# Kernel optimization log

Measured on AMD Instinct MI355X. Metric: run time of the kernel, lower is better.

## Reference

```python
import jax, jax.numpy as jnp
import numpy as np


def _matfun(X, f):
    """Apply scalar function f to eigenvalues of symmetric X (batched)."""
    Xs = 0.5 * (X + jnp.swapaxes(X, -1, -2))
    s, U = jnp.linalg.eigh(Xs)
    return jnp.einsum('...ij,...j,...kj->...ik', U, f(s), U)


def _invsqrtm(M):
    return _matfun(M, lambda s: 1.0 / jnp.sqrt(s))


def _sqrtm(M):
    return _matfun(M, jnp.sqrt)


def _logm(M):
    return _matfun(M, jnp.log)


def _expm(M):
    return _matfun(M, jnp.exp)


def _powm(M, p):
    return _matfun(M, lambda s: s ** p)


def setup_inputs() -> dict:
    key = jax.random.key(0)
    B, n = 2048, 128
    A = jax.random.normal(key, (B, n, n), dtype=jnp.float32)
    # SPD inputs: A A^T / n + 0.5 I (well conditioned, distinct eigenvalues)
    X = A @ jnp.swapaxes(A, -1, -2) / n + 0.5 * jnp.eye(n, dtype=jnp.float32)
    mean = jnp.eye(n, dtype=jnp.float32)          # self.mean (learn_mean=False)
    running_mean = jnp.eye(n, dtype=jnp.float32)  # running_mean buffer
    return {"X": X, "mean": mean, "running_mean": running_mean}


def reference(X, mean, running_mean):
    """SPDBatchNorm.forward, training mode, dispersion=False, batchdim=0."""
    karcher_steps = 1
    eta = 1.0
    sg = jax.lax.stop_gradient

    # Karcher flow to the batch Frechet mean
    batch_mean = X.mean(axis=0, keepdims=True)            # (1, n, n)
    for _ in range(karcher_steps):
        bm_invsqrt = _invsqrtm(sg(batch_mean))            # detach, as in torch
        X_proj = _logm(bm_invsqrt @ X @ bm_invsqrt)       # (B, n, n)
        bm_proj = X_proj.mean(axis=0, keepdims=True)
        bm_sqrt = _sqrtm(sg(batch_mean))
        batch_mean = bm_sqrt @ _expm(bm_proj) @ bm_sqrt

    # geodesic update of running mean toward batch mean (weight eta)
    rm_invsqrt = _invsqrtm(running_mean)
    power = _powm(rm_invsqrt @ batch_mean @ rm_invsqrt, eta)
    rm_sqrt = _sqrtm(running_mean)
    running_mean_new = rm_sqrt @ power @ rm_sqrt          # (1, n, n)

    # transp_via_identity(X, S=running_mean_new, T=mean):
    #   sqrt(T) @ invsqrt(S) @ X @ invsqrt(S) @ sqrt(T)
    S_invsqrt = _invsqrtm(running_mean_new)
    T_sqrt = _sqrtm(mean)
    Xn = T_sqrt @ (S_invsqrt @ X @ S_invsqrt) @ T_sqrt
    return Xn
```

## Files before the change

kernel.cpp:

```cpp
#include <hip/hip_runtime.h>

typedef _Float16 f16;
typedef _Float16 f16x8 __attribute__((ext_vector_type(8)));
typedef _Float16 f16x4 __attribute__((ext_vector_type(4)));
typedef float    f32x4 __attribute__((ext_vector_type(4)));

#define NN 16384

#define CHM 1.9f
#define CHH 1.6f
__device__ __constant__ float CB[14] = {
   0.6418302f,  0.8422835f, -0.3523330f,  0.1927408f,
  -0.1587888f,  0.1475312f,  0.1189440f, -0.2249536f,
  -0.4700032f,  0.5836800f,  0.4901376f, -0.5607424f,
  -0.2453504f,  0.2477460f };

__device__ __forceinline__ int swz(int r, int c) {
  return (r << 7) + ((((c >> 3) ^ (r & 7)) << 3) | (c & 7));
}

__device__ __forceinline__ void load_g2l_h(const f16* __restrict__ G, f16* buf, int t, int nt) {
  for (int ch = t; ch < 2048; ch += nt) {
    int r = ch >> 4, c8 = (ch & 15) << 3;
    *(f16x8*)(buf + swz(r, c8)) = *(const f16x8*)(G + (r << 7) + c8);
  }
}

__device__ __forceinline__ void stage32_512(const f16* __restrict__ src, f16* dst, int t) {
  const int w = t >> 6, l = t & 63;
  #pragma unroll
  for (int q = 0; q < 4; ++q) {
    const int cb = (w * 4 + q) * 64;
    __builtin_amdgcn_global_load_lds(
        (const __attribute__((address_space(1))) unsigned int*)(src + (size_t)(cb + l) * 8),
        (__attribute__((address_space(3))) unsigned int*)((char*)dst + (size_t)cb * 16), 16, 0, 0);
  }
}
__device__ __forceinline__ void stage32_256(const f16* __restrict__ src, f16* dst, int t) {
  const int w = t >> 6, l = t & 63;
  #pragma unroll
  for (int q = 0; q < 8; ++q) {
    const int cb = (w * 8 + q) * 64;
    __builtin_amdgcn_global_load_lds(
        (const __attribute__((address_space(1))) unsigned int*)(src + (size_t)(cb + l) * 8),
        (__attribute__((address_space(3))) unsigned int*)((char*)dst + (size_t)cb * 16), 16, 0, 0);
  }
}

template<int NI>
__device__ __forceinline__ void zero_acc(f32x4 (&acc)[NI][4]) {
  #pragma unroll
  for (int i = 0; i < NI; ++i)
    #pragma unroll
    for (int j = 0; j < 4; ++j) acc[i][j] = (f32x4){0.f, 0.f, 0.f, 0.f};
}

template<int NI>
__device__ __forceinline__ void mm_lds(const f16* A, const f16* Bh,
                                       f32x4 (&acc)[NI][4], int w, int l) {
  const int tr0 = (w >> 1) * (16 * NI), tc0 = (w & 1) * 64;
  #pragma unroll
  for (int ks = 0; ks < 4; ++ks) {
    const int kb = ks * 32 + ((l >> 4) << 3);
    f16x8 af[NI], bf[4];
    #pragma unroll
    for (int i = 0; i < NI; ++i) af[i] = *(const f16x8*)(A  + swz(tr0 + i*16 + (l & 15), kb));
    #pragma unroll
    for (int j = 0; j < 4; ++j) bf[j] = *(const f16x8*)(Bh + swz(tc0 + j*16 + (l & 15), kb));
    #pragma unroll
    for (int i = 0; i < NI; ++i)
      #pragma unroll
      for (int j = 0; j < 4; ++j)
        acc[i][j] = __builtin_amdgcn_mfma_f32_16x16x32_f16(af[i], bf[j], acc[i][j], 0, 0, 0);
  }
}

template<int NI>
__device__ __forceinline__ void mm_pre(const f16* A, const f16x8* bfr,
                                       f32x4 (&acc)[NI][4], int w, int l) {
  const int tr0 = (w >> 1) * (16 * NI);
  #pragma unroll
  for (int ks = 0; ks < 4; ++ks) {
    const int kb = ks * 32 + ((l >> 4) << 3);
    f16x8 af[NI];
    #pragma unroll
    for (int i = 0; i < NI; ++i) af[i] = *(const f16x8*)(A + swz(tr0 + i*16 + (l & 15), kb));
    #pragma unroll
    for (int i = 0; i < NI; ++i)
      #pragma unroll
      for (int j = 0; j < 4; ++j)
        acc[i][j] = __builtin_amdgcn_mfma_f32_16x16x32_f16(af[i], bfr[ks*4+j], acc[i][j], 0, 0, 0);
  }
}
__device__ __forceinline__ void pre_bf_gswz(const f16* __restrict__ B, f16x8* bfr, int w, int l) {
  const int tc0 = (w & 1) * 64;
  #pragma unroll
  for (int ks = 0; ks < 4; ++ks) {
    const int kb = ks * 32 + ((l >> 4) << 3);
    #pragma unroll
    for (int j = 0; j < 4; ++j)
      bfr[ks*4+j] = *(const f16x8*)(B + swz(tc0 + j*16 + (l & 15), kb));
  }
}
template<int NI>
__device__ __forceinline__ void pre_chunks(const f16* M, f16x4* Cc, int w, int l) {
  const int tr0 = (w >> 1) * (16 * NI), tc0 = (w & 1) * 64;
  #pragma unroll
  for (int i = 0; i < NI; ++i) {
    const int rowb = tr0 + i*16 + ((l >> 4) << 2);
    #pragma unroll
    for (int j = 0; j < 4; ++j)
      Cc[i*4+j] = *(const f16x4*)(M + swz(tc0 + j*16 + (l & 15), rowb));
  }
}

template<int NI>
__device__ __forceinline__ void wb_t(f16* buf, const f32x4 (&acc)[NI][4], int w, int l,
                                     float alpha, float beta) {
  const int tr0 = (w >> 1) * (16 * NI), tc0 = (w & 1) * 64;
  #pragma unroll
  for (int i = 0; i < NI; ++i) {
    const int rowb = tr0 + i*16 + ((l >> 4) << 2);
    #pragma unroll
    for (int j = 0; j < 4; ++j) {
      const int colg = tc0 + j*16 + (l & 15);
      f16x4 h;
      #pragma unroll
      for (int r = 0; r < 4; ++r) {
        float v = alpha * acc[i][j][r];
        if (rowb + r == colg) v += beta;
        h[r] = (f16)v;
      }
      *(f16x4*)(buf + swz(colg, rowb)) = h;
    }
  }
}

template<int NI>
__device__ __forceinline__ void wb_t_split(f16* bh, f16* bl, const f32x4 (&acc)[NI][4],
                                           int w, int l) {
  const int tr0 = (w >> 1) * (16 * NI), tc0 = (w & 1) * 64;
  #pragma unroll
  for (int i = 0; i < NI; ++i) {
    const int rowb = tr0 + i*16 + ((l >> 4) << 2);
    #pragma unroll
    for (int j = 0; j < 4; ++j) {
      const int colg = tc0 + j*16 + (l & 15);
      f16x4 hh, hl;
      #pragma unroll
      for (int r = 0; r < 4; ++r) {
        float v = acc[i][j][r];
        f16 hi = (f16)v;
        hh[r] = hi; hl[r] = (f16)(v - (float)hi);
      }
      *(f16x4*)(bh + swz(colg, rowb)) = hh;
      *(f16x4*)(bl + swz(colg, rowb)) = hl;
    }
  }
}

template<int NI>
__device__ __forceinline__ void wb_t_combo3L(f16* buf, const f32x4 (&acc)[NI][4],
                                             const f16x4* Uc, const f16x4* U2c, const f16* C3,
                                             int w, int l, float d0, float d1, float d2, float d3) {
  const int tr0 = (w >> 1) * (16 * NI), tc0 = (w & 1) * 64;
  #pragma unroll
  for (int i = 0; i < NI; ++i) {
    const int rowb = tr0 + i*16 + ((l >> 4) << 2);
    #pragma unroll
    for (int j = 0; j < 4; ++j) {
      const int colg = tc0 + j*16 + (l & 15);
      f16x4 c3 = *(const f16x4*)(C3 + swz(colg, rowb));
      f16x4 h;
      #pragma unroll
      for (int r = 0; r < 4; ++r) {
        float v = acc[i][j][r] + d1 * (float)Uc[i*4+j][r] + d2 * (float)U2c[i*4+j][r]
                               + d3 * (float)c3[r];
        if (rowb + r == colg) v += d0;
        h[r] = (f16)v;
      }
      *(f16x4*)(buf + swz(colg, rowb)) = h;
    }
  }
}

template<int NI>
__device__ __forceinline__ void wb_t_gc(f16* buf, const f32x4 (&acc)[NI][4],
                                        const f16* C1, const f16* C2,
                                        int w, int l, float d0, float d1, float d2) {
  const int tr0 = (w >> 1) * (16 * NI), tc0 = (w & 1) * 64;
  #pragma unroll
  for (int i = 0; i < NI; ++i) {
    const int rowb = tr0 + i*16 + ((l >> 4) << 2);
    #pragma unroll
    for (int j = 0; j < 4; ++j) {
      const int colg = tc0 + j*16 + (l & 15);
      f16x4 c1 = *(const f16x4*)(C1 + swz(colg, rowb));
      f16x4 c2 = *(const f16x4*)(C2 + swz(colg, rowb));
      f16x4 h;
      #pragma unroll
      for (int r = 0; r < 4; ++r) {
        float v = acc[i][j][r] + d1 * (float)c1[r] + d2 * (float)c2[r];
        if (rowb + r == colg) v += d0;
        h[r] = (f16)v;
      }
      *(f16x4*)(buf + swz(colg, rowb)) = h;
    }
  }
}

__global__ void k_mean_part(const float* __restrict__ X, f16* __restrict__ Xh,
                            float* __restrict__ part, int nper) {
  const int ch = blockIdx.x * 256 + threadIdx.x;
  const int bc = blockIdx.y;
  const int r = ch >> 4, c8 = (ch & 15) << 3;
  const int dsw = swz(r, c8);
  const float* p = X + (size_t)bc * nper * NN + (size_t)ch * 8;
  f16* xh = Xh + (size_t)bc * nper * NN + dsw;
  f32x4 s0 = {0.f,0.f,0.f,0.f}, s1 = {0.f,0.f,0.f,0.f};
  for (int b = 0; b < nper; ++b) {
    const float* g = p + (size_t)b * NN;
    f32x4 v0 = *(const f32x4*)g;
    f32x4 v1 = *(const f32x4*)(g + 4);
    s0 = s0 + v0; s1 = s1 + v1;
    f16x8 h;
    h[0]=(f16)v0[0]; h[1]=(f16)v0[1]; h[2]=(f16)v0[2]; h[3]=(f16)v0[3];
    h[4]=(f16)v1[0]; h[5]=(f16)v1[1]; h[6]=(f16)v1[2]; h[7]=(f16)v1[3];
    *(f16x8*)(xh + (size_t)b * NN) = h;
  }
  f32x4* pp = (f32x4*)(part + (size_t)bc * NN);
  pp[ch * 2]     = s0;
  pp[ch * 2 + 1] = s1;
}
__global__ void k_mean_fin(const float* __restrict__ part, float* __restrict__ M0, float scale) {
  int e4 = blockIdx.x * 256 + threadIdx.x;
  f32x4 s = {0.f,0.f,0.f,0.f};
  for (int c = 0; c < 32; ++c) s = s + ((const f32x4*)part)[(size_t)c * 4096 + e4];
  ((f32x4*)M0)[e4] = s * scale;
}

__global__ __launch_bounds__(512) void kB(
    const float* __restrict__ M0, f16* __restrict__ Cps,
    f16* __restrict__ Rh, f16* __restrict__ Rl) {
  __shared__ __align__(16) f16 A1[NN], A2[NN], A3[NN], A4[NN];
  __shared__ float red[128];
  __shared__ float sS;
  const int t = threadIdx.x, w = t >> 6, l = t & 63;
  if (t < 128) red[t] = M0[t * 129];
  __syncthreads();
  for (int s = 64; s > 0; s >>= 1) { if (t < s) red[t] += red[t + s]; __syncthreads(); }
  if (t == 0) sS = red[0] / 128.f;
  __syncthreads();
  const float s = sS, inv = 1.f / s;
  for (int e = t; e < NN; e += 512) {
    int r = e >> 7, c = e & 127;
    A1[swz(r, c)] = (f16)(M0[e] * inv - (r == c ? 1.f : 0.f));
  }
  __syncthreads();
  f32x4 acc[2][4];
  zero_acc<2>(acc); mm_lds<2>(A1, A1, acc, w, l); wb_t<2>(A2, acc, w, l, 1.f, 0.f); __syncthreads();
  zero_acc<2>(acc); mm_lds<2>(A2, A1, acc, w, l); wb_t<2>(A3, acc, w, l, 1.f, 0.f); __syncthreads();
  zero_acc<2>(acc); mm_lds<2>(A2, A2, acc, w, l); wb_t<2>(A4, acc, w, l, 1.f, 0.f); __syncthreads();
  const float rs = sqrtf(s), irs = 1.f / rs;
  for (int e = t; e < NN; e += 512) {
    int r = e >> 7, c = e & 127; int ix = swz(r, c);
    float a1 = (float)A1[ix], a2 = (float)A2[ix], a3 = (float)A3[ix], a4 = (float)A4[ix];
    float d = (r == c) ? 1.f : 0.f;
    float cp = (d - 0.5f*a1 + 0.375f*a2 - 0.3125f*a3 + 0.2734375f*a4) * irs;
    float rr = (d + 0.5f*a1 - 0.125f*a2 + 0.0625f*a3 - 0.0390625f*a4) * rs;
    Cps[ix] = (f16)cp;
    f16 rh = (f16)rr; Rh[e] = rh; Rl[e] = (f16)(rr - (float)rh);
  }
}

__global__ __launch_bounds__(512) void k_batch_log(
    const f16* __restrict__ Xh, const f16* __restrict__ Cps,
    float* __restrict__ Ppart, int per_blk) {
  __shared__ __align__(16) f16 S0[NN], S1[NN], S2[NN], S3[NN], S4[NN];
  const int t = threadIdx.x, w = t >> 6, l = t & 63;
  f32x4 lsum[2][4]; zero_acc<2>(lsum);
  f32x4 acc[2][4];
  for (int m = 0; m < per_blk; ++m) {
    const size_t b = (size_t)blockIdx.x * per_blk + m;
    if (m == 0) stage32_512(Xh + b * NN, S0, t);
    stage32_512(Cps, S2, t);
    asm volatile("s_waitcnt vmcnt(0)" ::: "memory");
    __syncthreads();
    if (m > 0) {
      for (int g = t; g < 2048; g += 512)
        *(f16x8*)(S0 + g * 8) = *(const f16x8*)(S4 + g * 8);
    }
    __syncthreads();
    zero_acc<2>(acc); mm_lds<2>(S0, S2, acc, w, l);
    wb_t<2>(S1, acc, w, l, 1.f, 0.f); __syncthreads();
    zero_acc<2>(acc); mm_lds<2>(S1, S2, acc, w, l);
    wb_t<2>(S0, acc, w, l, 1.f / CHH, -CHM / CHH); __syncthreads();
    zero_acc<2>(acc); mm_lds<2>(S0, S0, acc, w, l); wb_t<2>(S2, acc, w, l, 1.f, 0.f); __syncthreads();
    zero_acc<2>(acc); mm_lds<2>(S2, S0, acc, w, l); wb_t<2>(S3, acc, w, l, 1.f, 0.f); __syncthreads();
    zero_acc<2>(acc); mm_lds<2>(S2, S2, acc, w, l); wb_t<2>(S1, acc, w, l, 1.f, 0.f); __syncthreads();
    f16x4 Uc[8], U2c[8];
    pre_chunks<2>(S0, Uc, w, l);
    pre_chunks<2>(S2, U2c, w, l);
    __syncthreads();
    for (int g = t; g < 2048; g += 512) {
      int e0 = g * 8;
      f16x8 u = *(const f16x8*)(S0 + e0);
      int r = e0 >> 7;
      int c0 = ((((e0 >> 3) & 15) ^ (r & 7)) << 3);
      f16x8 h;
      #pragma unroll
      for (int k = 0; k < 8; ++k) {
        float v = CB[13] * (float)u[k];
        if (r == c0 + k) v += CB[12];
        h[k] = (f16)v;
      }
      *(f16x8*)(S0 + e0) = h;
    }
    __syncthreads();
    if (m + 1 < per_blk) stage32_512(Xh + (b + 1) * NN, S4, t);
    f16* pc = S0; f16* pn = S2;
    #pragma unroll
    for (int jj = 2; jj >= 1; --jj) {
      zero_acc<2>(acc);
      mm_lds<2>(pc, S1, acc, w, l);
      wb_t_combo3L<2>(pn, acc, Uc, U2c, S3, w, l,
                      CB[4*jj], CB[4*jj+1], CB[4*jj+2], CB[4*jj+3]);
      __syncthreads();
      f16* tmp = pc; pc = pn; pn = tmp;
    }
    zero_acc<2>(acc);
    mm_lds<2>(pc, S1, acc, w, l);
    {
      const int tr0 = (w >> 1) * 32, tc0 = (w & 1) * 64;
      #pragma unroll
      for (int i = 0; i < 2; ++i) {
        const int rowb = tr0 + i*16 + ((l >> 4) << 2);
        #pragma unroll
        for (int j = 0; j < 4; ++j) {
          const int colg = tc0 + j*16 + (l & 15);
          f16x4 c3 = *(const f16x4*)(S3 + swz(colg, rowb));
          #pragma unroll
          for (int r = 0; r < 4; ++r) {
            float v = acc[i][j][r] + CB[1] * (float)Uc[i*4+j][r]
                    + CB[2] * (float)U2c[i*4+j][r] + CB[3] * (float)c3[r];
            if (rowb + r == colg) v += CB[0];
            lsum[i][j][r] += v;
          }
        }
      }
    }
    __syncthreads();
  }
  float* pp = Ppart + (size_t)blockIdx.x * NN;
  const int tr0 = (w >> 1) * 32, tc0 = (w & 1) * 64;
  #pragma unroll
  for (int i = 0; i < 2; ++i) {
    const int rowb = tr0 + i*16 + ((l >> 4) << 2);
    #pragma unroll
    for (int j = 0; j < 4; ++j) {
      const int colg = tc0 + j*16 + (l & 15);
      *(f32x4*)(pp + colg * 128 + rowb) = lsum[i][j];
    }
  }
}

__global__ void k_reduceP(const float* __restrict__ Pp, float* __restrict__ P, float invBn) {
  int e4 = blockIdx.x * 256 + threadIdx.x;
  f32x4 s = {0.f, 0.f, 0.f, 0.f};
  for (int b = 0; b < 256; ++b) s = s + ((const f32x4*)Pp)[(size_t)b * 4096 + e4];
  ((f32x4*)P)[e4] = s * invBn;
}

__global__ __launch_bounds__(512) void kD(
    const float* __restrict__ P, const float* __restrict__ mean,
    const f16* __restrict__ Rh, const f16* __restrict__ Rl,
    f16* __restrict__ Gs) {
  __shared__ __align__(16) f16 B1[NN], B2[NN], B3[NN], B4[NN];
  __shared__ float red[128];
  __shared__ float sv;
  const int t = threadIdx.x, w = t >> 6, l = t & 63;
  f32x4 acc[2][4];
  if (t < 128) red[t] = P[t * 129];
  __syncthreads();
  for (int s = 64; s > 0; s >>= 1) { if (t < s) red[t] += red[t + s]; __syncthreads(); }
  if (t == 0) sv = red[0] / 128.f;
  __syncthreads();
  const float mu = sv;
  for (int e = t; e < NN; e += 512) {
    int r = e >> 7, c = e & 127;
    B1[swz(r, c)] = (f16)(P[e] - (r == c ? mu : 0.f));
  }
  __syncthreads();
  zero_acc<2>(acc); mm_lds<2>(B1, B1, acc, w, l); wb_t<2>(B2, acc, w, l, 1.f, 0.f); __syncthreads();
  zero_acc<2>(acc); mm_lds<2>(B2, B1, acc, w, l); wb_t<2>(B3, acc, w, l, 1.f, 0.f); __syncthreads();
  for (int g = t; g < 2048; g += 512) {
    int e0 = g * 8;
    f16x8 d1 = *(const f16x8*)(B1 + e0);
    f16x8 d2 = *(const f16x8*)(B2 + e0);
    int r = e0 >> 7;
    int c0 = ((((e0 >> 3) & 15) ^ (r & 7)) << 3);
    f16x8 h;
    #pragma unroll
    for (int k = 0; k < 8; ++k) {
      float v = (1.f/5040.f) * (float)d1[k] + (1.f/40320.f) * (float)d2[k];
      if (r == c0 + k) v += (1.f/720.f);
      h[k] = (f16)v;
    }
    *(f16x8*)(B4 + e0) = h;
  }
  __syncthreads();
  zero_acc<2>(acc); mm_lds<2>(B3, B4, acc, w, l); __syncthreads();
  wb_t_gc<2>(B4, acc, B1, B2, w, l, 1.f/6.f, 1.f/24.f, 1.f/120.f);
  __syncthreads();
  zero_acc<2>(acc); mm_lds<2>(B3, B4, acc, w, l); __syncthreads();
  {
    const float emu = expf(mu);
    const int tr0 = (w >> 1) * 32, tc0 = (w & 1) * 64;
    #pragma unroll
    for (int i = 0; i < 2; ++i) {
      const int rowb = tr0 + i*16 + ((l >> 4) << 2);
      #pragma unroll
      for (int j = 0; j < 4; ++j) {
        const int colg = tc0 + j*16 + (l & 15);
        f16x4 dc  = *(const f16x4*)(B1 + swz(colg, rowb));
        f16x4 d2c = *(const f16x4*)(B2 + swz(colg, rowb));
        f16x4 hh, hl;
        #pragma unroll
        for (int r = 0; r < 4; ++r) {
          float v = acc[i][j][r] + (float)dc[r] + 0.5f * (float)d2c[r];
          if (rowb + r == colg) v += 1.f;
          v *= emu;
          f16 hi = (f16)v; hh[r] = hi; hl[r] = (f16)(v - (float)hi);
        }
        *(f16x4*)(B2 + swz(colg, rowb)) = hh;
        *(f16x4*)(B3 + swz(colg, rowb)) = hl;
      }
    }
  }
  __syncthreads();
  load_g2l_h(Rh, B1, t, 512);
  load_g2l_h(Rl, B4, t, 512);
  __syncthreads();
  zero_acc<2>(acc);
  mm_lds<2>(B2, B1, acc, w, l);
  mm_lds<2>(B2, B4, acc, w, l);
  mm_lds<2>(B3, B1, acc, w, l);
  __syncthreads();
  wb_t_split<2>(B2, B3, acc, w, l);
  __syncthreads();
  zero_acc<2>(acc);
  mm_lds<2>(B1, B2, acc, w, l);
  mm_lds<2>(B1, B3, acc, w, l);
  mm_lds<2>(B4, B2, acc, w, l);
  __syncthreads();
  wb_t_split<2>(B2, B3, acc, w, l);
  __syncthreads();
  if (t < 128) red[t] = (float)B2[swz(t, t)] + (float)B3[swz(t, t)];
  __syncthreads();
  for (int s = 64; s > 0; s >>= 1) { if (t < s) red[t] += red[t + s]; __syncthreads(); }
  if (t == 0) sv = red[0] / 128.f;
  __syncthreads();
  const float s2 = sv, inv2 = 1.f / s2;
  for (int e = t; e < NN; e += 512) {
    int r = e >> 7, c = e & 127; int ix = swz(r, c);
    B1[ix] = (f16)(((float)B2[ix] + (float)B3[ix]) * inv2 - (r == c ? 1.f : 0.f));
  }
  __syncthreads();
  zero_acc<2>(acc); mm_lds<2>(B1, B1, acc, w, l); wb_t<2>(B4, acc, w, l, 1.f, 0.f); __syncthreads();
  zero_acc<2>(acc); mm_lds<2>(B4, B1, acc, w, l); wb_t<2>(B2, acc, w, l, 1.f, 0.f); __syncthreads();
  zero_acc<2>(acc); mm_lds<2>(B4, B4, acc, w, l); wb_t<2>(B3, acc, w, l, 1.f, 0.f); __syncthreads();
  {
    const float is2 = 1.f / sqrtf(s2);
    for (int e = t; e < NN; e += 512) {
      int r = e >> 7, c = e & 127; int ix = swz(r, c);
      float f1 = (float)B1[ix], f2 = (float)B4[ix], f3 = (float)B2[ix], f4 = (float)B3[ix];
      float d = (r == c) ? 1.f : 0.f;
      float vv = (d - 0.5f*f1 + 0.375f*f2 - 0.3125f*f3 + 0.2734375f*f4) * is2;
      f16 hi = (f16)vv;
      B1[ix] = hi; B4[ix] = (f16)(vv - (float)hi);
    }
  }
  __syncthreads();
  if (t < 128) red[t] = mean[t * 129];
  __syncthreads();
  for (int s = 64; s > 0; s >>= 1) { if (t < s) red[t] += red[t + s]; __syncthreads(); }
  if (t == 0) sv = red[0] / 128.f;
  __syncthreads();
  const float s3 = sv, inv3 = 1.f / s3;
  for (int e = t; e < NN; e += 512) {
    int r = e >> 7, c = e & 127;
    B2[swz(r, c)] = (f16)(mean[e] * inv3 - (r == c ? 1.f : 0.f));
  }
  __syncthreads();
  zero_acc<2>(acc); mm_lds<2>(B2, B2, acc, w, l); __syncthreads();
  wb_t<2>(B3, acc, w, l, 1.f, 0.f); __syncthreads();
  {
    const float rs3 = sqrtf(s3);
    for (int e = t; e < NN; e += 512) {
      int r = e >> 7, c = e & 127; int ix = swz(r, c);
      float m1 = (float)B2[ix], m2 = (float)B3[ix];
      float d = (r == c) ? 1.f : 0.f;
      float vv = (d + 0.5f*m1 - 0.125f*m2) * rs3;
      f16 hi = (f16)vv;
      B2[ix] = hi; B3[ix] = (f16)(vv - (float)hi);
    }
  }
  __syncthreads();
  zero_acc<2>(acc);
  mm_lds<2>(B1, B2, acc, w, l);
  mm_lds<2>(B1, B3, acc, w, l);
  mm_lds<2>(B4, B2, acc, w, l);
  {
    const int tr0 = (w >> 1) * 32, tc0 = (w & 1) * 64;
    #pragma unroll
    for (int i = 0; i < 2; ++i) {
      const int rowb = tr0 + i*16 + ((l >> 4) << 2);
      #pragma unroll
      for (int j = 0; j < 4; ++j) {
        const int colg = tc0 + j*16 + (l & 15);
        f16x4 h;
        #pragma unroll
        for (int r = 0; r < 4; ++r) h[r] = (f16)acc[i][j][r];
        *(f16x4*)(Gs + swz(colg, rowb)) = h;
      }
    }
  }
}

__global__ __launch_bounds__(256, 1) void k_apply(
    const f16* __restrict__ Xh, const f16* __restrict__ Gs,
    float* __restrict__ Out, int per_blk) {
  __shared__ __align__(16) f16 SX[NN], ST[NN];
  const int t = threadIdx.x, w = t >> 6, l = t & 63;
  f16x8 bg[16];
  pre_bf_gswz(Gs, bg, w, l);
  f32x4 acc[4][4];
  for (int m = 0; m < per_blk; ++m) {
    const size_t b = (size_t)blockIdx.x * per_blk + m;
    stage32_256(Xh + b * NN, SX, t);
    asm volatile("s_waitcnt vmcnt(0)" ::: "memory");
    __syncthreads();
    zero_acc<4>(acc); mm_pre<4>(SX, bg, acc, w, l); __syncthreads();
    wb_t<4>(ST, acc, w, l, 1.f, 0.f); __syncthreads();
    zero_acc<4>(acc); mm_pre<4>(ST, bg, acc, w, l);
    float* O = Out + b * NN;
    const int tr0 = (w >> 1) * 64, tc0 = (w & 1) * 64;
    #pragma unroll
    for (int i = 0; i < 4; ++i) {
      const int rowb = tr0 + i*16 + ((l >> 4) << 2);
      #pragma unroll
      for (int j = 0; j < 4; ++j) {
        const int colg = tc0 + j*16 + (l & 15);
        *(f32x4*)(O + colg * 128 + rowb) = acc[i][j];
      }
    }
    __syncthreads();
  }
}

extern "C" void kernel_launch(void* const* d_in, const int* in_sizes, int n_in,
                              void* d_out, int out_size, void* d_ws, size_t ws_size,
                              hipStream_t stream) {
  const float* X    = (const float*)d_in[0];
  const float* mean = (const float*)d_in[1];
  const int Bn = in_sizes[0] / NN;

  float* wsf = (float*)d_ws;
  float* M0 = wsf;
  float* P  = wsf + NN;
  f16* hbase = (f16*)(wsf + 2 * (size_t)NN);
  f16 *Cps = hbase;
  f16 *Rh  = hbase + NN, *Rl = hbase + 2 * NN;
  f16 *Gs  = hbase + 3 * NN;
  float* Ppart = wsf + 4 * (size_t)NN;
  f16* Xh = (f16*)(wsf + (4 + 256) * (size_t)NN);

  k_mean_part<<<dim3(8, 32), 256, 0, stream>>>(X, Xh, Ppart, Bn / 32);
  k_mean_fin<<<16, 256, 0, stream>>>(Ppart, M0, 1.f / (float)Bn);
  kB<<<1, 512, 0, stream>>>(M0, Cps, Rh, Rl);
  k_batch_log<<<256, 512, 0, stream>>>(Xh, Cps, Ppart, Bn / 256);
  k_reduceP<<<16, 256, 0, stream>>>(Ppart, P, 1.f / (float)Bn);
  kD<<<1, 512, 0, stream>>>(P, mean, Rh, Rl, Gs);
  k_apply<<<512, 256, 0, stream>>>(Xh, Gs, (float*)d_out, Bn / 512);
}
```

Before: 270.7 us.

## Shorten log polynomial, drop prefetch buffer, widen single-block kernels to 1024 threads

The Chebyshev-style log polynomial in the batch kernel is refit with fewer coefficients. This removes one of the high-degree matrix-multiply stages per matrix and folds more terms into the elementwise initialisation. The separate prefetch buffer S4 and its copy-back are dropped, and the next matrix is staged directly into S0 once S0 is no longer needed. The two single-block setup kernels (kB, kD) now run with 1024 threads and half the tile per wave to shorten their serial latency. Accuracy of the log approximation may drop, and prefetch overlap is reduced.

```diff
diff --git a/kernel.cpp b/kernel.cpp
--- a/kernel.cpp
+++ b/kernel.cpp
@@ -9,11 +9,10 @@
 
 #define CHM 1.9f
 #define CHH 1.6f
-__device__ __constant__ float CB[14] = {
-   0.6418302f,  0.8422835f, -0.3523330f,  0.1927408f,
-  -0.1587888f,  0.1475312f,  0.1189440f, -0.2249536f,
-  -0.4700032f,  0.5836800f,  0.4901376f, -0.5607424f,
-  -0.2453504f,  0.2477460f };
+__device__ __constant__ float CB[12] = {
+   0.6419309f,  0.8414791f, -0.3609340f,  0.2147234f,
+  -0.0582120f, -0.0285232f, -0.3102016f,  0.3787296f,
+   0.3577728f, -0.4226304f, -0.2457600f,  0.2444390f };
 
 __device__ __forceinline__ int swz(int r, int c) {
   return (r << 7) + ((((c >> 3) ^ (r & 7)) << 3) | (c & 7));
@@ -239,7 +238,7 @@
   ((f32x4*)M0)[e4] = s * scale;
 }
 
-__global__ __launch_bounds__(512) void kB(
+__global__ __launch_bounds__(1024) void kB(
     const float* __restrict__ M0, f16* __restrict__ Cps,
     f16* __restrict__ Rh, f16* __restrict__ Rl) {
   __shared__ __align__(16) f16 A1[NN], A2[NN], A3[NN], A4[NN];
@@ -252,17 +251,17 @@
   if (t == 0) sS = red[0] / 128.f;
   __syncthreads();
   const float s = sS, inv = 1.f / s;
-  for (int e = t; e < NN; e += 512) {
+  for (int e = t; e < NN; e += 1024) {
     int r = e >> 7, c = e & 127;
     A1[swz(r, c)] = (f16)(M0[e] * inv - (r == c ? 1.f : 0.f));
   }
   __syncthreads();
-  f32x4 acc[2][4];
-  zero_acc<2>(acc); mm_lds<2>(A1, A1, acc, w, l); wb_t<2>(A2, acc, w, l, 1.f, 0.f); __syncthreads();
-  zero_acc<2>(acc); mm_lds<2>(A2, A1, acc, w, l); wb_t<2>(A3, acc, w, l, 1.f, 0.f); __syncthreads();
-  zero_acc<2>(acc); mm_lds<2>(A2, A2, acc, w, l); wb_t<2>(A4, acc, w, l, 1.f, 0.f); __syncthreads();
+  f32x4 acc[1][4];
+  zero_acc<1>(acc); mm_lds<1>(A1, A1, acc, w, l); wb_t<1>(A2, acc, w, l, 1.f, 0.f); __syncthreads();
+  zero_acc<1>(acc); mm_lds<1>(A2, A1, acc, w, l); wb_t<1>(A3, acc, w, l, 1.f, 0.f); __syncthreads();
+  zero_acc<1>(acc); mm_lds<1>(A2, A2, acc, w, l); wb_t<1>(A4, acc, w, l, 1.f, 0.f); __syncthreads();
   const float rs = sqrtf(s), irs = 1.f / rs;
-  for (int e = t; e < NN; e += 512) {
+  for (int e = t; e < NN; e += 1024) {
     int r = e >> 7, c = e & 127; int ix = swz(r, c);
     float a1 = (float)A1[ix], a2 = (float)A2[ix], a3 = (float)A3[ix], a4 = (float)A4[ix];
     float d = (r == c) ? 1.f : 0.f;
@@ -276,7 +275,7 @@
 __global__ __launch_bounds__(512) void k_batch_log(
     const f16* __restrict__ Xh, const f16* __restrict__ Cps,
     float* __restrict__ Ppart, int per_blk) {
-  __shared__ __align__(16) f16 S0[NN], S1[NN], S2[NN], S3[NN], S4[NN];
+  __shared__ __align__(16) f16 S0[NN], S1[NN], S2[NN], S3[NN];
   const int t = threadIdx.x, w = t >> 6, l = t & 63;
   f32x4 lsum[2][4]; zero_acc<2>(lsum);
   f32x4 acc[2][4];
@@ -285,11 +284,6 @@
     if (m == 0) stage32_512(Xh + b * NN, S0, t);
     stage32_512(Cps, S2, t);
     asm volatile("s_waitcnt vmcnt(0)" ::: "memory");
-    __syncthreads();
-    if (m > 0) {
-      for (int g = t; g < 2048; g += 512)
-        *(f16x8*)(S0 + g * 8) = *(const f16x8*)(S4 + g * 8);
-    }
     __syncthreads();
     zero_acc<2>(acc); mm_lds<2>(S0, S2, acc, w, l);
     wb_t<2>(S1, acc, w, l, 1.f, 0.f); __syncthreads();
@@ -304,32 +298,28 @@
     __syncthreads();
     for (int g = t; g < 2048; g += 512) {
       int e0 = g * 8;
-      f16x8 u = *(const f16x8*)(S0 + e0);
+      f16x8 u  = *(const f16x8*)(S0 + e0);
+      f16x8 u2 = *(const f16x8*)(S2 + e0);
+      f16x8 u3 = *(const f16x8*)(S3 + e0);
       int r = e0 >> 7;
       int c0 = ((((e0 >> 3) & 15) ^ (r & 7)) << 3);
       f16x8 h;
       #pragma unroll
       for (int k = 0; k < 8; ++k) {
-        float v = CB[13] * (float)u[k];
-        if (r == c0 + k) v += CB[12];
+        float v = CB[9] * (float)u[k] + CB[10] * (float)u2[k] + CB[11] * (float)u3[k];
+        if (r == c0 + k) v += CB[8];
         h[k] = (f16)v;
       }
       *(f16x8*)(S0 + e0) = h;
     }
     __syncthreads();
-    if (m + 1 < per_blk) stage32_512(Xh + (b + 1) * NN, S4, t);
-    f16* pc = S0; f16* pn = S2;
-    #pragma unroll
-    for (int jj = 2; jj >= 1; --jj) {
-      zero_acc<2>(acc);
-      mm_lds<2>(pc, S1, acc, w, l);
-      wb_t_combo3L<2>(pn, acc, Uc, U2c, S3, w, l,
-                      CB[4*jj], CB[4*jj+1], CB[4*jj+2], CB[4*jj+3]);
-      __syncthreads();
-      f16* tmp = pc; pc = pn; pn = tmp;
-    }
     zero_acc<2>(acc);
-    mm_lds<2>(pc, S1, acc, w, l);
+    mm_lds<2>(S0, S1, acc, w, l);
+    wb_t_combo3L<2>(S2, acc, Uc, U2c, S3, w, l, CB[4], CB[5], CB[6], CB[7]);
+    __syncthreads();
+    if (m + 1 < per_blk) stage32_512(Xh + (b + 1) * NN, S0, t);
+    zero_acc<2>(acc);
+    mm_lds<2>(S2, S1, acc, w, l);
     {
       const int tr0 = (w >> 1) * 32, tc0 = (w & 1) * 64;
       #pragma unroll
@@ -371,7 +361,7 @@
   ((f32x4*)P)[e4] = s * invBn;
 }
 
-__global__ __launch_bounds__(512) void kD(
+__global__ __launch_bounds__(1024) void kD(
     const float* __restrict__ P, const float* __restrict__ mean,
     const f16* __restrict__ Rh, const f16* __restrict__ Rl,
     f16* __restrict__ Gs) {
@@ -379,21 +369,21 @@
   __shared__ float red[128];
   __shared__ float sv;
   const int t = threadIdx.x, w = t >> 6, l = t & 63;
-  f32x4 acc[2][4];
+  f32x4 acc[1][4];
   if (t < 128) red[t] = P[t * 129];
   __syncthreads();
   for (int s = 64; s > 0; s >>= 1) { if (t < s) red[t] += red[t + s]; __syncthreads(); }
   if (t == 0) sv = red[0] / 128.f;
   __syncthreads();
   const float mu = sv;
-  for (int e = t; e < NN; e += 512) {
+  for (int e = t; e < NN; e += 1024) {
     int r = e >> 7, c = e & 127;
     B1[swz(r, c)] = (f16)(P[e] - (r == c ? mu : 0.f));
   }
   __syncthreads();
-  zero_acc<2>(acc); mm_lds<2>(B1, B1, acc, w, l); wb_t<2>(B2, acc, w, l, 1.f, 0.f); __syncthreads();
-  zero_acc<2>(acc); mm_lds<2>(B2, B1, acc, w, l); wb_t<2>(B3, acc, w, l, 1.f, 0.f); __syncthreads();
-  for (int g = t; g < 2048; g += 512) {
+  zero_acc<1>(acc); mm_lds<1>(B1, B1, acc, w, l); wb_t<1>(B2, acc, w, l, 1.f, 0.f); __syncthreads();
+  zero_acc<1>(acc); mm_lds<1>(B2, B1, acc, w, l); wb_t<1>(B3, acc, w, l, 1.f, 0.f); __syncthreads();
+  for (int g = t; g < 2048; g += 1024) {
     int e0 = g * 8;
     f16x8 d1 = *(const f16x8*)(B1 + e0);
     f16x8 d2 = *(const f16x8*)(B2 + e0);
@@ -409,51 +399,48 @@
     *(f16x8*)(B4 + e0) = h;
   }
   __syncthreads();
-  zero_acc<2>(acc); mm_lds<2>(B3, B4, acc, w, l); __syncthreads();
-  wb_t_gc<2>(B4, acc, B1, B2, w, l, 1.f/6.f, 1.f/24.f, 1.f/120.f);
-  __syncthreads();
-  zero_acc<2>(acc); mm_lds<2>(B3, B4, acc, w, l); __syncthreads();
+  zero_acc<1>(acc); mm_lds<1>(B3, B4, acc, w, l); __syncthreads();
+  wb_t_gc<1>(B4, acc, B1, B2, w, l, 1.f/6.f, 1.f/24.f, 1.f/120.f);
+  __syncthreads();
+  zero_acc<1>(acc); mm_lds<1>(B3, B4, acc, w, l); __syncthreads();
   {
     const float emu = expf(mu);
-    const int tr0 = (w >> 1) * 32, tc0 = (w & 1) * 64;
-    #pragma unroll
-    for (int i = 0; i < 2; ++i) {
-      const int rowb = tr0 + i*16 + ((l >> 4) << 2);
-      #pragma unroll
-      for (int j = 0; j < 4; ++j) {
-        const int colg = tc0 + j*16 + (l & 15);
-        f16x4 dc  = *(const f16x4*)(B1 + swz(colg, rowb));
-        f16x4 d2c = *(const f16x4*)(B2 + swz(colg, rowb));
-        f16x4 hh, hl;
-        #pragma unroll
-        for (int r = 0; r < 4; ++r) {
-          float v = acc[i][j][r] + (float)dc[r] + 0.5f * (float)d2c[r];
-          if (rowb + r == colg) v += 1.f;
-          v *= emu;
-          f16 hi = (f16)v; hh[r] = hi; hl[r] = (f16)(v - (float)hi);
-        }
-        *(f16x4*)(B2 + swz(colg, rowb)) = hh;
-        *(f16x4*)(B3 + swz(colg, rowb)) = hl;
-      }
-    }
-  }
-  __syncthreads();
-  load_g2l_h(Rh, B1, t, 512);
-  load_g2l_h(Rl, B4, t, 512);
-  __syncthreads();
-  zero_acc<2>(acc);
-  mm_lds<2>(B2, B1, acc, w, l);
-  mm_lds<2>(B2, B4, acc, w, l);
-  mm_lds<2>(B3, B1, acc, w, l);
-  __syncthreads();
-  wb_t_split<2>(B2, B3, acc, w, l);
-  __syncthreads();
-  zero_acc<2>(acc);
-  mm_lds<2>(B1, B2, acc, w, l);
-  mm_lds<2>(B1, B3, acc, w, l);
-  mm_lds<2>(B4, B2, acc, w, l);
-  __syncthreads();
-  wb_t_split<2>(B2, B3, acc, w, l);
+    const int rowb = (w >> 1) * 16 + ((l >> 4) << 2);
+    const int tc0  = (w & 1) * 64;
+    #pragma unroll
+    for (int j = 0; j < 4; ++j) {
+      const int colg = tc0 + j*16 + (l & 15);
+      f16x4 dc  = *(const f16x4*)(B1 + swz(colg, rowb));
+      f16x4 d2c = *(const f16x4*)(B2 + swz(colg, rowb));
+      f16x4 hh, hl;
+      #pragma unroll
+      for (int r = 0; r < 4; ++r) {
+        float v = acc[0][j][r] + (float)dc[r] + 0.5f * (float)d2c[r];
+        if (rowb + r == colg) v += 1.f;
+        v *= emu;
+        f16 hi = (f16)v; hh[r] = hi; hl[r] = (f16)(v - (float)hi);
+      }
+      *(f16x4*)(B2 + swz(colg, rowb)) = hh;
+      *(f16x4*)(B3 + swz(colg, rowb)) = hl;
+    }
+  }
+  __syncthreads();
+  load_g2l_h(Rh, B1, t, 1024);
+  load_g2l_h(Rl, B4, t, 1024);
+  __syncthreads();
+  zero_acc<1>(acc);
+  mm_lds<1>(B2, B1, acc, w, l);
+  mm_lds<1>(B2, B4, acc, w, l);
+  mm_lds<1>(B3, B1, acc, w, l);
+  __syncthreads();
+  wb_t_split<1>(B2, B3, acc, w, l);
+  __syncthreads();
+  zero_acc<1>(acc);
+  mm_lds<1>(B1, B2, acc, w, l);
+  mm_lds<1>(B1, B3, acc, w, l);
+  mm_lds<1>(B4, B2, acc, w, l);
+  __syncthreads();
+  wb_t_split<1>(B2, B3, acc, w, l);
   __syncthreads();
   if (t < 128) red[t] = (float)B2[swz(t, t)] + (float)B3[swz(t, t)];
   __syncthreads();
@@ -461,17 +448,17 @@
   if (t == 0) sv = red[0] / 128.f;
   __syncthreads();
   const float s2 = sv, inv2 = 1.f / s2;
-  for (int e = t; e < NN; e += 512) {
+  for (int e = t; e < NN; e += 1024) {
     int r = e >> 7, c = e & 127; int ix = swz(r, c);
     B1[ix] = (f16)(((float)B2[ix] + (float)B3[ix]) * inv2 - (r == c ? 1.f : 0.f));
   }
   __syncthreads();
-  zero_acc<2>(acc); mm_lds<2>(B1, B1, acc, w, l); wb_t<2>(B4, acc, w, l, 1.f, 0.f); __syncthreads();
-  zero_acc<2>(acc); mm_lds<2>(B4, B1, acc, w, l); wb_t<2>(B2, acc, w, l, 1.f, 0.f); __syncthreads();
-  zero_acc<2>(acc); mm_lds<2>(B4, B4, acc, w, l); wb_t<2>(B3, acc, w, l, 1.f, 0.f); __syncthreads();
+  zero_acc<1>(acc); mm_lds<1>(B1, B1, acc, w, l); wb_t<1>(B4, acc, w, l, 1.f, 0.f); __syncthreads();
+  zero_acc<1>(acc); mm_lds<1>(B4, B1, acc, w, l); wb_t<1>(B2, acc, w, l, 1.f, 0.f); __syncthreads();
+  zero_acc<1>(acc); mm_lds<1>(B4, B4, acc, w, l); wb_t<1>(B3, acc, w, l, 1.f, 0.f); __syncthreads();
   {
     const float is2 = 1.f / sqrtf(s2);
-    for (int e = t; e < NN; e += 512) {
+    for (int e = t; e < NN; e += 1024) {
       int r = e >> 7, c = e & 127; int ix = swz(r, c);
       float f1 = (float)B1[ix], f2 = (float)B4[ix], f3 = (float)B2[ix], f4 = (float)B3[ix];
       float d = (r == c) ? 1.f : 0.f;
@@ -487,16 +474,16 @@
   if (t == 0) sv = red[0] / 128.f;
   __syncthreads();
   const float s3 = sv, inv3 = 1.f / s3;
-  for (int e = t; e < NN; e += 512) {
+  for (int e = t; e < NN; e += 1024) {
     int r = e >> 7, c = e & 127;
     B2[swz(r, c)] = (f16)(mean[e] * inv3 - (r == c ? 1.f : 0.f));
   }
   __syncthreads();
-  zero_acc<2>(acc); mm_lds<2>(B2, B2, acc, w, l); __syncthreads();
-  wb_t<2>(B3, acc, w, l, 1.f, 0.f); __syncthreads();
+  zero_acc<1>(acc); mm_lds<1>(B2, B2, acc, w, l); __syncthreads();
+  wb_t<1>(B3, acc, w, l, 1.f, 0.f); __syncthreads();
   {
     const float rs3 = sqrtf(s3);
-    for (int e = t; e < NN; e += 512) {
+    for (int e = t; e < NN; e += 1024) {
       int r = e >> 7, c = e & 127; int ix = swz(r, c);
       float m1 = (float)B2[ix], m2 = (float)B3[ix];
       float d = (r == c) ? 1.f : 0.f;
@@ -506,23 +493,20 @@
     }
   }
   __syncthreads();
-  zero_acc<2>(acc);
-  mm_lds<2>(B1, B2, acc, w, l);
-  mm_lds<2>(B1, B3, acc, w, l);
-  mm_lds<2>(B4, B2, acc, w, l);
+  zero_acc<1>(acc);
+  mm_lds<1>(B1, B2, acc, w, l);
+  mm_lds<1>(B1, B3, acc, w, l);
+  mm_lds<1>(B4, B2, acc, w, l);
   {
-    const int tr0 = (w >> 1) * 32, tc0 = (w & 1) * 64;
-    #pragma unroll
-    for (int i = 0; i < 2; ++i) {
-      const int rowb = tr0 + i*16 + ((l >> 4) << 2);
-      #pragma unroll
-      for (int j = 0; j < 4; ++j) {
-        const int colg = tc0 + j*16 + (l & 15);
-        f16x4 h;
-        #pragma unroll
-        for (int r = 0; r < 4; ++r) h[r] = (f16)acc[i][j][r];
-        *(f16x4*)(Gs + swz(colg, rowb)) = h;
-      }
+    const int rowb = (w >> 1) * 16 + ((l >> 4) << 2);
+    const int tc0  = (w & 1) * 64;
+    #pragma unroll
+    for (int j = 0; j < 4; ++j) {
+      const int colg = tc0 + j*16 + (l & 15);
+      f16x4 h;
+      #pragma unroll
+      for (int r = 0; r < 4; ++r) h[r] = (f16)acc[0][j][r];
+      *(f16x4*)(Gs + swz(colg, rowb)) = h;
     }
   }
 }
@@ -577,9 +561,9 @@
 
   k_mean_part<<<dim3(8, 32), 256, 0, stream>>>(X, Xh, Ppart, Bn / 32);
   k_mean_fin<<<16, 256, 0, stream>>>(Ppart, M0, 1.f / (float)Bn);
-  kB<<<1, 512, 0, stream>>>(M0, Cps, Rh, Rl);
+  kB<<<1, 1024, 0, stream>>>(M0, Cps, Rh, Rl);
   k_batch_log<<<256, 512, 0, stream>>>(Xh, Cps, Ppart, Bn / 256);
   k_reduceP<<<16, 256, 0, stream>>>(Ppart, P, 1.f / (float)Bn);
-  kD<<<1, 512, 0, stream>>>(P, mean, Rh, Rl, Gs);
+  kD<<<1, 1024, 0, stream>>>(P, mean, Rh, Rl, Gs);
   k_apply<<<512, 256, 0, stream>>>(Xh, Gs, (float*)d_out, Bn / 512);
 }
```

New measurement: 280.7 us. +3.7%, slower.
